# Kernel optimization log

Hardware: AMD Instinct MI355X
Metric: run time of the kernel (lower is better)

Reference implementation:

```python
import jax, jax.numpy as jnp
import numpy as np

D = 512        # input_dim
T = 64         # n_trees
DEPTH = 3
NI = 2 ** DEPTH - 1   # 7 internal nodes
NL = 2 ** DEPTH       # 8 leaves
PPT = NI * D + NI + NL * 2   # params per tree
TOT = PPT * T + T            # + tree_weights
HID = 64


def setup_inputs() -> dict:
    key = jax.random.key(0)
    ks = jax.random.split(key, 10)
    w = lambda k, s: jax.random.normal(k, s, jnp.float32) * 0.05  # xavier-ish small gain
    return {
        "X_train": jax.random.normal(ks[0], (8192, D), jnp.float32),
        "X_test": jax.random.normal(ks[1], (32768, D), jnp.float32),
        "y_train": jax.random.randint(ks[2], (8192,), 0, 2, jnp.int64),
        "W1": w(ks[3], (HID, D)), "b1": jnp.zeros(HID), "g1": jnp.ones(HID), "be1": jnp.zeros(HID),
        "W2": w(ks[4], (HID, HID)), "b2": jnp.zeros(HID),
        "H1": w(ks[5], (2 * HID, HID)), "hb1": jnp.zeros(2 * HID),
        "g2": jnp.ones(2 * HID), "be2": jnp.zeros(2 * HID),
        "H2": w(ks[6], (2 * HID, 2 * HID)), "hb2": jnp.zeros(2 * HID),
        "H3": w(ks[7], (TOT, 2 * HID)), "hb3": jnp.zeros(TOT),
    }


def _ln(x, g, b, eps=1e-5):
    m = x.mean(-1, keepdims=True)
    v = ((x - m) ** 2).mean(-1, keepdims=True)
    return (x - m) / jnp.sqrt(v + eps) * g + b


def reference(X_train, X_test, y_train, W1, b1, g1, be1, W2, b2,
              H1, hb1, g2, be2, H2, hb2, H3, hb3):
    # --- hypernet: data encoder + param generator (Dropout is eval=identity) ---
    h = jax.nn.relu(_ln(X_train @ W1.T + b1, g1, be1))
    h = jax.nn.relu(h @ W2.T + b2)
    c = h.mean(axis=0)                              # [HID] context
    u = jax.nn.relu(_ln(c @ H1.T + hb1, g2, be2))
    u = jax.nn.relu(u @ H2.T + hb2)
    params = u @ H3.T + hb3                         # [TOT]

    # --- parse per-tree params (sequential layout) ---
    rows = params[: T * PPT].reshape(T, PPT)
    sw = rows[:, : NI * D].reshape(T, NI, D)        # split weights
    sb = rows[:, NI * D: NI * D + NI]               # split bias [T, NI]
    ll = rows[:, NI * D + NI:].reshape(T, NL, 2)    # leaf logits
    tw = params[T * PPT:]                           # tree weights [T]

    # --- soft decision trees, all trees/nodes batched ---
    # sigmoid split prob for every (sample, tree, internal node); temperature=1
    p = jax.nn.sigmoid(jnp.einsum('bd,tnd->btn', X_test, sw) + sb[None])  # [B,T,NI]
    B = X_test.shape[0]
    lp = jnp.ones((B, T, 1), X_test.dtype)
    for d in range(DEPTH):                          # unrolled fixed-depth traversal
        s = 2 ** d - 1                              # heap offset of level d
        pd = p[:, :, s: s + 2 ** d]                 # [B,T,2^d]
        lp = jnp.stack([lp * (1 - pd), lp * pd], axis=-1).reshape(B, T, 2 ** (d + 1))
    # original code adds leaf contributions twice (main loop + cleanup loop)
    lp = lp * 2.0                                   # [B,T,NL]

    leaf_dist = jax.nn.softmax(ll, axis=-1)         # [T,NL,2]
    out_t = jnp.einsum('btl,tlc->btc', lp, leaf_dist)
    w = jax.nn.softmax(tw, axis=0)                  # [T]
    return jnp.einsum('btc,t->bc', out_t, w)        # [B,2]
```

## Files before the change

### kernel.cpp

```cpp
#include <hip/hip_runtime.h>
#include <hip/hip_bf16.h>

#define DD 512
#define HIDN 64
#define NTREE 64
#define NIN 7
#define PPTC 3607
#define TOTP 230912
#define SWROWS 448

typedef __attribute__((ext_vector_type(8))) short bf16x8;
typedef __attribute__((ext_vector_type(4))) float f32x4;
typedef __attribute__((ext_vector_type(8))) _Float16 h16x8;

__device__ __forceinline__ unsigned short f2bf(float f) {
  unsigned u = __float_as_uint(f);
  unsigned r = (u + 0x7FFFu + ((u >> 16) & 1u)) >> 16;
  return (unsigned short)r;
}
__device__ __forceinline__ float sigmoidf_(float x) {
  return 1.0f / (1.0f + __expf(-x));
}
__device__ __forceinline__ uint2 pack_bf16x4(float4 v) {
  uint2 pk;
  pk.x = (unsigned)f2bf(v.x) | ((unsigned)f2bf(v.y) << 16);
  pk.y = (unsigned)f2bf(v.z) | ((unsigned)f2bf(v.w) << 16);
  return pk;
}
__device__ __forceinline__ bf16x8 cvt8(float4 a, float4 b) {
  unsigned u0, u1, u2, u3;
  asm("v_cvt_pk_bf16_f32 %0, %1, %2" : "=v"(u0) : "v"(a.x), "v"(a.y));
  asm("v_cvt_pk_bf16_f32 %0, %1, %2" : "=v"(u1) : "v"(a.z), "v"(a.w));
  asm("v_cvt_pk_bf16_f32 %0, %1, %2" : "=v"(u2) : "v"(b.x), "v"(b.y));
  asm("v_cvt_pk_bf16_f32 %0, %1, %2" : "=v"(u3) : "v"(b.z), "v"(b.w));
  union { unsigned u[4]; bf16x8 v; } r;
  r.u[0] = u0; r.u[1] = u1; r.u[2] = u2; r.u[3] = u3;
  return r.v;
}
__device__ __forceinline__ void gl_lds16(const void* g, void* l) {
  __builtin_amdgcn_global_load_lds(
      (const __attribute__((address_space(1))) unsigned int*)g,
      (__attribute__((address_space(3))) unsigned int*)l, 16, 0, 0);
}

__global__ __launch_bounds__(256) void k_train(
    const float* __restrict__ Xtr, const float* __restrict__ W1,
    const float* __restrict__ b1, const float* __restrict__ g1,
    const float* __restrict__ be1, const float* __restrict__ W2,
    const float* __restrict__ b2, float* __restrict__ c_part)
{
  __shared__ __align__(16) char smem[37888];
  char* Xc  = smem;
  char* W1c = smem + 8192;
  char* Hl  = smem + 24576;
  char* W2l = smem + 28672;
  float* lnb = (float*)(smem + 36864);
  float* cp  = (float*)(smem + 37376);

  const int tid = threadIdx.x;
  const int lane = tid & 63;
  const int wv = tid >> 6;
  const int l15 = lane & 15;
  const int gq = lane >> 4;
  const int wm = wv >> 1;
  const int wn = wv & 1;
  const int rb0 = blockIdx.x * 32;

  const float4* X4g = (const float4*)Xtr;
  const float4* W4g = (const float4*)W1;

#pragma unroll
  for (int s = 0; s < 4; ++s) {
    int fidx = tid + s * 256;
    int n = fidx >> 4, kq = fidx & 15;
    float4 v = ((const float4*)W2)[n * 16 + kq];
    uint2 pk = pack_bf16x4(v);
    int off = n * 128 + kq * 8; off ^= (n & 7) << 4;
    *(uint2*)(W2l + off) = pk;
  }

  int xga[4], xo[4];
#pragma unroll
  for (int s = 0; s < 4; ++s) {
    int f = tid + s * 256;
    int m = f >> 5, kq = f & 31;
    xga[s] = (rb0 + m) * 128 + kq;
    xo[s] = (m * 256 + kq * 8) ^ ((m & 7) << 4);
  }
  int wga[8], wo[8];
#pragma unroll
  for (int s = 0; s < 8; ++s) {
    int f = tid + s * 256;
    int n = f >> 5, kq = f & 31;
    wga[s] = n * 128 + kq;
    wo[s] = (n * 256 + kq * 8) ^ ((n & 7) << 4);
  }

  f32x4 acc1[2];
#pragma unroll
  for (int nt = 0; nt < 2; ++nt) { f32x4 z = {0.f,0.f,0.f,0.f}; acc1[nt] = z; }

  float4 xr[4], wr[8];
#pragma unroll
  for (int s = 0; s < 4; ++s) xr[s] = X4g[xga[s]];
#pragma unroll
  for (int s = 0; s < 8; ++s) wr[s] = W4g[wga[s]];

  for (int kc = 0; kc < 4; ++kc) {
    __syncthreads();
#pragma unroll
    for (int s = 0; s < 4; ++s) *(uint2*)(Xc + xo[s]) = pack_bf16x4(xr[s]);
#pragma unroll
    for (int s = 0; s < 8; ++s) *(uint2*)(W1c + wo[s]) = pack_bf16x4(wr[s]);
    if (kc < 3) {
      int ko = (kc + 1) * 32;
#pragma unroll
      for (int s = 0; s < 4; ++s) xr[s] = X4g[xga[s] + ko];
#pragma unroll
      for (int s = 0; s < 8; ++s) wr[s] = W4g[wga[s] + ko];
    }
    __syncthreads();
#pragma unroll
    for (int ks = 0; ks < 4; ++ks) {
      int arow = wm * 16 + l15;
      int aoff = (arow * 256 + ks * 64 + gq * 16) ^ ((arow & 7) << 4);
      bf16x8 afr = *(const bf16x8*)(Xc + aoff);
#pragma unroll
      for (int nt = 0; nt < 2; ++nt) {
        int brow = wn * 32 + nt * 16 + l15;
        int boff = (brow * 256 + ks * 64 + gq * 16) ^ ((brow & 7) << 4);
        bf16x8 bfr = *(const bf16x8*)(W1c + boff);
        acc1[nt] = __builtin_amdgcn_mfma_f32_16x16x32_bf16(afr, bfr, acc1[nt], 0, 0, 0);
      }
    }
  }

  float b1v[2], g1v[2], be1v[2], b2v[2];
#pragma unroll
  for (int nt = 0; nt < 2; ++nt) {
    int c = wn * 32 + nt * 16 + l15;
    b1v[nt] = b1[c]; g1v[nt] = g1[c]; be1v[nt] = be1[c]; b2v[nt] = b2[c];
  }
  float yv[2][4], s_[4], q_[4];
#pragma unroll
  for (int i = 0; i < 4; ++i) {
    float s = 0.f, q = 0.f;
#pragma unroll
    for (int nt = 0; nt < 2; ++nt) {
      float y = acc1[nt][i] + b1v[nt];
      yv[nt][i] = y; s += y; q += y * y;
    }
    s_[i] = s; q_[i] = q;
  }
#pragma unroll
  for (int off = 1; off < 16; off <<= 1) {
#pragma unroll
    for (int i = 0; i < 4; ++i) {
      s_[i] += __shfl_xor(s_[i], off);
      q_[i] += __shfl_xor(q_[i], off);
    }
  }
  if (l15 == 0) {
#pragma unroll
    for (int i = 0; i < 4; ++i) {
      int row = wm * 16 + gq * 4 + i;
      float2 sv; sv.x = s_[i]; sv.y = q_[i];
      *(float2*)(lnb + (row * 2 + wn) * 2) = sv;
    }
  }
  __syncthreads();
#pragma unroll
  for (int i = 0; i < 4; ++i) {
    int row = wm * 16 + gq * 4 + i;
    float2 e0 = *(float2*)(lnb + (row * 2 + 0) * 2);
    float2 e1 = *(float2*)(lnb + (row * 2 + 1) * 2);
    float m = (e0.x + e1.x) * (1.0f / 64.0f);
    float var = (e0.y + e1.y) * (1.0f / 64.0f) - m * m;
    float rstd = rsqrtf(var + 1e-5f);
#pragma unroll
    for (int nt = 0; nt < 2; ++nt) {
      float h = (yv[nt][i] - m) * rstd * g1v[nt] + be1v[nt];
      h = fmaxf(h, 0.0f);
      int col = wn * 32 + nt * 16 + l15;
      int off2 = (row * 128 + col * 2) ^ ((row & 7) << 4);
      *(unsigned short*)(Hl + off2) = f2bf(h);
    }
  }
  __syncthreads();

  f32x4 acc2[2];
#pragma unroll
  for (int nt = 0; nt < 2; ++nt) { f32x4 z = {0.f,0.f,0.f,0.f}; acc2[nt] = z; }
#pragma unroll
  for (int ks = 0; ks < 2; ++ks) {
    int arow = wm * 16 + l15;
    int aoff = (arow * 128 + ks * 64 + gq * 16) ^ ((arow & 7) << 4);
    bf16x8 afr = *(const bf16x8*)(Hl + aoff);
#pragma unroll
    for (int nt = 0; nt < 2; ++nt) {
      int brow = wn * 32 + nt * 16 + l15;
      int boff = (brow * 128 + ks * 64 + gq * 16) ^ ((brow & 7) << 4);
      bf16x8 bfr = *(const bf16x8*)(W2l + boff);
      acc2[nt] = __builtin_amdgcn_mfma_f32_16x16x32_bf16(afr, bfr, acc2[nt], 0, 0, 0);
    }
  }
  float cs[2];
#pragma unroll
  for (int nt = 0; nt < 2; ++nt) {
    float s = 0.f;
#pragma unroll
    for (int i = 0; i < 4; ++i) s += fmaxf(acc2[nt][i] + b2v[nt], 0.0f);
    cs[nt] = s;
  }
#pragma unroll
  for (int nt = 0; nt < 2; ++nt) {
    cs[nt] += __shfl_xor(cs[nt], 16);
    cs[nt] += __shfl_xor(cs[nt], 32);
  }
  if (lane < 16) {
#pragma unroll
    for (int nt = 0; nt < 2; ++nt)
      cp[wm * 64 + wn * 32 + nt * 16 + lane] = cs[nt];
  }
  __syncthreads();
  if (tid < 64) c_part[blockIdx.x * 64 + tid] = cp[tid] + cp[64 + tid];
}

__global__ __launch_bounds__(256) void k_head(
    const float* __restrict__ c_part,
    const float* __restrict__ H1, const float* __restrict__ hb1,
    const float* __restrict__ g2, const float* __restrict__ be2,
    const float* __restrict__ H2, const float* __restrict__ hb2,
    float* __restrict__ u2out)
{
  __shared__ float part[256];
  __shared__ float clds[64];
  __shared__ float u1lds[128];
  __shared__ float red[8];
  int tid = threadIdx.x;
  {
    int col = tid & 63, g = tid >> 6;
    float s0 = 0.f, s1 = 0.f, s2 = 0.f, s3 = 0.f;
    int b0 = g * 64;
    for (int b = 0; b < 64; b += 4) {
      s0 += c_part[(b0 + b + 0) * 64 + col];
      s1 += c_part[(b0 + b + 1) * 64 + col];
      s2 += c_part[(b0 + b + 2) * 64 + col];
      s3 += c_part[(b0 + b + 3) * 64 + col];
    }
    part[tid] = (s0 + s1) + (s2 + s3);
  }
  __syncthreads();
  if (tid < 64)
    clds[tid] = (part[tid] + part[64 + tid] + part[128 + tid] + part[192 + tid]) * (1.0f / 8192.0f);
  __syncthreads();
  float acc = 0.f;
  if (tid < 128) {
    float a0 = 0.f, a1 = 0.f, a2 = 0.f, a3 = 0.f;
    for (int k = 0; k < 64; k += 4) {
      a0 += clds[k + 0] * H1[tid * 64 + k + 0];
      a1 += clds[k + 1] * H1[tid * 64 + k + 1];
      a2 += clds[k + 2] * H1[tid * 64 + k + 2];
      a3 += clds[k + 3] * H1[tid * 64 + k + 3];
    }
    acc = hb1[tid] + ((a0 + a1) + (a2 + a3));
  }
  float s = acc, q = acc * acc;
#pragma unroll
  for (int off = 1; off < 64; off <<= 1) { s += __shfl_xor(s, off); q += __shfl_xor(q, off); }
  int wv = tid >> 6;
  if ((tid & 63) == 0) { red[wv * 2] = s; red[wv * 2 + 1] = q; }
  __syncthreads();
  float S = red[0] + red[2], Q = red[1] + red[3];
  float m = S * (1.0f / 128.0f);
  float var = Q * (1.0f / 128.0f) - m * m;
  float rstd = rsqrtf(var + 1e-5f);
  if (tid < 128)
    u1lds[tid] = fmaxf((acc - m) * rstd * g2[tid] + be2[tid], 0.0f);
  __syncthreads();
  if (tid < 128) {
    float c0 = 0.f, c1 = 0.f, c2 = 0.f, c3 = 0.f;
    for (int k = 0; k < 128; k += 4) {
      c0 += u1lds[k + 0] * H2[tid * 128 + k + 0];
      c1 += u1lds[k + 1] * H2[tid * 128 + k + 1];
      c2 += u1lds[k + 2] * H2[tid * 128 + k + 2];
      c3 += u1lds[k + 3] * H2[tid * 128 + k + 3];
    }
    u2out[tid] = fmaxf(hb2[tid] + ((c0 + c1) + (c2 + c3)), 0.0f);
  }
}

__global__ __launch_bounds__(256) void k_params(
    const float* __restrict__ H3, const float* __restrict__ hb3,
    const float* __restrict__ u2,
    unsigned short* __restrict__ Bfrag, float* __restrict__ sb,
    float* __restrict__ ll, float* __restrict__ tw)
{
  __shared__ float u2l[128];
  int tid = threadIdx.x;
  if (tid < 128) u2l[tid] = u2[tid];
  __syncthreads();
  int row = blockIdx.x * 64 + (tid >> 2);
  int sub = tid & 3;
  float acc = 0.0f;
  const float4* H4 = (const float4*)H3;
#pragma unroll
  for (int j = 0; j < 8; ++j) {
    int f = j * 4 + sub;
    float4 v = H4[row * 32 + f];
    acc += v.x * u2l[f * 4] + v.y * u2l[f * 4 + 1] + v.z * u2l[f * 4 + 2] + v.w * u2l[f * 4 + 3];
  }
  acc += __shfl_xor(acc, 1);
  acc += __shfl_xor(acc, 2);
  if (sub == 0) {
    float val = acc + hb3[row];
    if (row >= 230848) {
      tw[row - 230848] = val;
    } else {
      int t = row / PPTC;
      int r = row - t * PPTC;
      if (r < 3584) {
        int n = r >> 9, d = r & 511;
        int col = t * 7 + n;
        int kt = d >> 5, gq = (d >> 3) & 3, j = d & 7;
        Bfrag[kt * 16384 + col * 32 + (gq ^ (col & 3)) * 8 + j] = f2bf(val);
      } else if (r < 3591) {
        sb[t * 7 + (r - 3584)] = val;
      } else {
        ll[t * 16 + (r - 3591)] = val;
      }
    }
  }
}

__global__ __launch_bounds__(512) void k_test(
    const float* __restrict__ Xt, const unsigned short* __restrict__ Bfrag,
    const float* __restrict__ sb, const float* __restrict__ ll,
    const float* __restrict__ tw, float* __restrict__ out)
{
  __shared__ __align__(16) char smem[154368];
  char* Pl = smem;
  float* qlds = (float*)(smem + 147456);
  float* sbl  = (float*)(smem + 151552);
  float* outl = (float*)(smem + 153344);

  const int tid = threadIdx.x;
  const int lane = tid & 63;
  const int wv = tid >> 6;
  const int l15 = lane & 15;
  const int gq = lane >> 4;
  const int wm = wv >> 2;
  const int wn = wv & 3;
  const int bm0 = blockIdx.x * 128;

  const float4* X4 = (const float4*)Xt;
  const char* Bf = (const char*)Bfrag;

  if (tid < 448) sbl[tid] = sb[tid];
  if (tid < 64) {
    int t = tid;
    float x = tw[t];
    float m = x;
#pragma unroll
    for (int off = 1; off < 64; off <<= 1) m = fmaxf(m, __shfl_xor(m, off));
    float e = __expf(x - m);
    float s = e;
#pragma unroll
    for (int off = 1; off < 64; off <<= 1) s += __shfl_xor(s, off);
    float w = e / s;
#pragma unroll
    for (int l = 0; l < 8; ++l) {
      float a = ll[t * 16 + l * 2], b = ll[t * 16 + l * 2 + 1];
      float mm = fmaxf(a, b);
      float e0 = __expf(a - mm), e1 = __expf(b - mm);
      float inv = 2.0f * w / (e0 + e1);
      qlds[t * 16 + l * 2] = e0 * inv;
      qlds[t * 16 + l * 2 + 1] = e1 * inv;
    }
  }

  const int xrow0 = tid >> 3;
  const int xpg   = (tid & 7) ^ (xrow0 & 7);
  const int xsrc0 = (bm0 + xrow0) * 128 + xpg;
  const int xsrc1 = (bm0 + xrow0 + 64) * 128 + xpg;

#define ISSUE_TILE(t_) do { \
    char* xb_ = smem + ((t_) % 3) * 49152; \
    char* bb_ = xb_ + 16384; \
    gl_lds16(X4 + (xsrc0 + (t_) * 8), xb_ + tid * 16); \
    gl_lds16(X4 + (xsrc1 + (t_) * 8), xb_ + (tid + 512) * 16); \
    const char* bt_ = Bf + (t_) * 32768; \
    gl_lds16(bt_ + tid * 16,          bb_ + tid * 16); \
    gl_lds16(bt_ + (tid + 512) * 16,  bb_ + (tid + 512) * 16); \
    gl_lds16(bt_ + (tid + 1024) * 16, bb_ + (tid + 1024) * 16); \
    gl_lds16(bt_ + (tid + 1536) * 16, bb_ + (tid + 1536) * 16); \
  } while (0)

  f32x4 acc[4][7];
#pragma unroll
  for (int mt = 0; mt < 4; ++mt)
#pragma unroll
    for (int nt = 0; nt < 7; ++nt) { f32x4 z = {0.f,0.f,0.f,0.f}; acc[mt][nt] = z; }

  const int xoff0 = (((gq * 2) ^ (l15 & 7)) << 4);
  const int xoff1 = (((gq * 2 + 1) ^ (l15 & 7)) << 4);
  int arow[4];
#pragma unroll
  for (int mt = 0; mt < 4; ++mt) arow[mt] = (wm * 64 + mt * 16 + l15) * 128;
  const int bxor = ((gq ^ (l15 & 3)) << 4);
  int boffs[7];
#pragma unroll
  for (int nt = 0; nt < 7; ++nt) boffs[nt] = (wn * 112 + nt * 16 + l15) * 64 + bxor;

#define COMPUTE_TILE(t_) do { \
    char* xb_ = smem + ((t_) % 3) * 49152; \
    char* bb_ = xb_ + 16384; \
    bf16x8 abf[4]; \
    _Pragma("unroll") \
    for (int mt = 0; mt < 4; ++mt) { \
      float4 a0 = *(const float4*)(xb_ + arow[mt] + xoff0); \
      float4 a1 = *(const float4*)(xb_ + arow[mt] + xoff1); \
      abf[mt] = cvt8(a0, a1); \
    } \
    _Pragma("unroll") \
    for (int nt = 0; nt < 7; ++nt) { \
      bf16x8 bfr = *(const bf16x8*)(bb_ + boffs[nt]); \
      _Pragma("unroll") \
      for (int mt = 0; mt < 4; ++mt) \
        acc[mt][nt] = __builtin_amdgcn_mfma_f32_16x16x32_bf16(abf[mt], bfr, acc[mt][nt], 0, 0, 0); \
    } } while (0)

  ISSUE_TILE(0);
  ISSUE_TILE(1);
  ISSUE_TILE(2);
  asm volatile("s_waitcnt lgkmcnt(0)" ::: "memory");

  for (int t = 0; t < 13; ++t) {
    asm volatile("s_waitcnt vmcnt(12)" ::: "memory");
    __builtin_amdgcn_sched_barrier(0);
    __builtin_amdgcn_s_barrier();
    COMPUTE_TILE(t);
    __builtin_amdgcn_s_barrier();
    ISSUE_TILE(t + 3);
  }
  asm volatile("s_waitcnt vmcnt(12)" ::: "memory");
  __builtin_amdgcn_sched_barrier(0);
  __builtin_amdgcn_s_barrier();
  COMPUTE_TILE(13);
  __builtin_amdgcn_s_barrier();
  asm volatile("s_waitcnt vmcnt(6)" ::: "memory");
  __builtin_amdgcn_sched_barrier(0);
  __builtin_amdgcn_s_barrier();
  COMPUTE_TILE(14);
  __builtin_amdgcn_s_barrier();
  asm volatile("s_waitcnt vmcnt(0)" ::: "memory");
  __builtin_amdgcn_sched_barrier(0);
  __builtin_amdgcn_s_barrier();
  COMPUTE_TILE(15);
  __syncthreads();

  float qreg[16];
  {
    const float4* q4 = (const float4*)qlds;
#pragma unroll
    for (int j = 0; j < 4; ++j) {
      float4 v = q4[lane * 4 + j];
      qreg[j * 4] = v.x; qreg[j * 4 + 1] = v.y; qreg[j * 4 + 2] = v.z; qreg[j * 4 + 3] = v.w;
    }
  }

#pragma unroll
  for (int rg = 0; rg < 4; ++rg) {
    if (wm == (rg >> 1)) {
#pragma unroll
      for (int mtl = 0; mtl < 2; ++mtl) {
        const int mt = (rg & 1) * 2 + mtl;
#pragma unroll
        for (int nt = 0; nt < 7; ++nt) {
          int col = wn * 112 + nt * 16 + l15;
          float sbv = sbl[col];
          int t = col / 7;
          int j = col - t * 7;
          int slot2 = (t * 8 + j) * 2;
#pragma unroll
          for (int i = 0; i < 4; ++i) {
            int rl = mtl * 16 + gq * 4 + i;
            float p = sigmoidf_(acc[mt][nt][i] + sbv);
            *(_Float16*)(Pl + rl * 1024 + slot2) = (_Float16)p;
          }
        }
      }
    }
    __syncthreads();
#pragma unroll
    for (int k = 0; k < 4; ++k) {
      int rl = wv * 4 + k;
      h16x8 v = *(const h16x8*)(Pl + rl * 1024 + lane * 16);
      float p0 = (float)v[0], p1 = (float)v[1], p2 = (float)v[2];
      float p3 = (float)v[3], p4 = (float)v[4], p5 = (float)v[5], p6 = (float)v[6];
      float n0 = 1.f - p0, n1 = 1.f - p1, n2 = 1.f - p2;
      float a00 = n0 * n1, a01 = n0 * p1, a10 = p0 * n2, a11 = p0 * p2;
      float L0 = a00 * (1.f - p3), L1 = a00 * p3;
      float L2 = a01 * (1.f - p4), L3 = a01 * p4;
      float L4 = a10 * (1.f - p5), L5 = a10 * p5;
      float L6 = a11 * (1.f - p6), L7 = a11 * p6;
      float o0 = L0*qreg[0] + L1*qreg[2] + L2*qreg[4] + L3*qreg[6]
               + L4*qreg[8] + L5*qreg[10] + L6*qreg[12] + L7*qreg[14];
      float o1 = L0*qreg[1] + L1*qreg[3] + L2*qreg[5] + L3*qreg[7]
               + L4*qreg[9] + L5*qreg[11] + L6*qreg[13] + L7*qreg[15];
#pragma unroll
      for (int off = 1; off < 64; off <<= 1) {
        o0 += __shfl_xor(o0, off);
        o1 += __shfl_xor(o1, off);
      }
      if (lane == 0) {
        int gr = rg * 32 + rl;
        outl[gr * 2] = o0;
        outl[gr * 2 + 1] = o1;
      }
    }
    __syncthreads();
  }
  if (tid < 256) out[bm0 * 2 + tid] = outl[tid];
#undef ISSUE_TILE
#undef COMPUTE_TILE
}

extern "C" void kernel_launch(void* const* d_in, const int* in_sizes, int n_in,
                              void* d_out, int out_size, void* d_ws, size_t ws_size,
                              hipStream_t stream)
{
  const float* Xtr = (const float*)d_in[0];
  const float* Xte = (const float*)d_in[1];
  const float* W1  = (const float*)d_in[3];
  const float* b1  = (const float*)d_in[4];
  const float* g1  = (const float*)d_in[5];
  const float* be1 = (const float*)d_in[6];
  const float* W2  = (const float*)d_in[7];
  const float* b2  = (const float*)d_in[8];
  const float* H1  = (const float*)d_in[9];
  const float* hb1 = (const float*)d_in[10];
  const float* g2  = (const float*)d_in[11];
  const float* be2 = (const float*)d_in[12];
  const float* H2  = (const float*)d_in[13];
  const float* hb2 = (const float*)d_in[14];
  const float* H3  = (const float*)d_in[15];
  const float* hb3 = (const float*)d_in[16];
  float* out = (float*)d_out;
  char* ws = (char*)d_ws;

  float* c_part = (float*)ws;
  float* u2     = (float*)(ws + 65536);
  float* sb     = (float*)(ws + 66048);
  float* ll     = (float*)(ws + 67840);
  float* tw     = (float*)(ws + 71936);
  unsigned short* Bfrag = (unsigned short*)(ws + 72192);

  k_train<<<256, 256, 0, stream>>>(Xtr, W1, b1, g1, be1, W2, b2, c_part);
  k_head<<<1, 256, 0, stream>>>(c_part, H1, hb1, g2, be2, H2, hb2, u2);
  k_params<<<3608, 256, 0, stream>>>(H3, hb3, u2, Bfrag, sb, ll, tw);
  k_test<<<256, 512, 0, stream>>>(Xte, Bfrag, sb, ll, tw, out);
}
```

Before: 84.53 us.

## Split test GEMM across tree halves with atomic output accumulation

The test kernel now splits the 448 split-node columns into two halves of 32 trees each. It launches 512 blocks of 256 threads instead of 256 blocks of 512, with a smaller double-buffered LDS footprint so two blocks can share a CU. Each block atomically adds its partial per-sample outputs into a buffer zeroed in k_params, and the B fragment layout is reorganised per half. The aim is better occupancy and CU balance, at the cost of reading X twice, atomic traffic, and a shallower prefetch pipeline.

```diff
diff --git a/kernel.cpp b/kernel.cpp
--- a/kernel.cpp
+++ b/kernel.cpp
@@ -294,11 +294,13 @@
     const float* __restrict__ H3, const float* __restrict__ hb3,
     const float* __restrict__ u2,
     unsigned short* __restrict__ Bfrag, float* __restrict__ sb,
-    float* __restrict__ ll, float* __restrict__ tw)
+    float* __restrict__ ll, float* __restrict__ tw,
+    float* __restrict__ outz)
 {
   __shared__ float u2l[128];
   int tid = threadIdx.x;
   if (tid < 128) u2l[tid] = u2[tid];
+  if (blockIdx.x < 256) outz[blockIdx.x * 256 + tid] = 0.0f;
   __syncthreads();
   int row = blockIdx.x * 64 + (tid >> 2);
   int sub = tid & 3;
@@ -321,9 +323,10 @@
       int r = row - t * PPTC;
       if (r < 3584) {
         int n = r >> 9, d = r & 511;
-        int col = t * 7 + n;
-        int kt = d >> 5, gq = (d >> 3) & 3, j = d & 7;
-        Bfrag[kt * 16384 + col * 32 + (gq ^ (col & 3)) * 8 + j] = f2bf(val);
+        int half = t >> 5;
+        int colp = (t & 31) * 7 + n;
+        int kt = d >> 5, kgq = (d >> 3) & 3, j = d & 7;
+        Bfrag[(half * 16 + kt) * 8192 + (kgq * 256 + colp) * 8 + j] = f2bf(val);
       } else if (r < 3591) {
         sb[t * 7 + (r - 3584)] = val;
       } else {
@@ -333,30 +336,33 @@
   }
 }
 
-__global__ __launch_bounds__(512) void k_test(
+__global__ __launch_bounds__(256, 2) void k_test(
     const float* __restrict__ Xt, const unsigned short* __restrict__ Bfrag,
     const float* __restrict__ sb, const float* __restrict__ ll,
     const float* __restrict__ tw, float* __restrict__ out)
 {
-  __shared__ __align__(16) char smem[154368];
+  __shared__ __align__(16) char smem[68608];
   char* Pl = smem;
-  float* qlds = (float*)(smem + 147456);
-  float* sbl  = (float*)(smem + 151552);
-  float* outl = (float*)(smem + 153344);
+  float* qlds = (float*)(smem + 65536);
+  float* sbl  = (float*)(smem + 67584);
 
   const int tid = threadIdx.x;
   const int lane = tid & 63;
   const int wv = tid >> 6;
   const int l15 = lane & 15;
   const int gq = lane >> 4;
-  const int wm = wv >> 2;
-  const int wn = wv & 3;
-  const int bm0 = blockIdx.x * 128;
+  const int wm = wv >> 1;
+  const int wn = wv & 1;
+  const int bx = blockIdx.x;
+  const int mblk = (bx >> 4) * 8 + (bx & 7);
+  const int half = (bx >> 3) & 1;
+  const int bm0 = mblk * 128;
+  const int T0 = half * 32;
 
   const float4* X4 = (const float4*)Xt;
-  const char* Bf = (const char*)Bfrag;
-
-  if (tid < 448) sbl[tid] = sb[tid];
+  const char* Bf = (const char*)Bfrag + half * 262144;
+
+  if (tid < 224) sbl[tid] = sb[T0 * 7 + tid];
   if (tid < 64) {
     int t = tid;
     float x = tw[t];
@@ -368,32 +374,40 @@
 #pragma unroll
     for (int off = 1; off < 64; off <<= 1) s += __shfl_xor(s, off);
     float w = e / s;
-#pragma unroll
-    for (int l = 0; l < 8; ++l) {
-      float a = ll[t * 16 + l * 2], b = ll[t * 16 + l * 2 + 1];
-      float mm = fmaxf(a, b);
-      float e0 = __expf(a - mm), e1 = __expf(b - mm);
-      float inv = 2.0f * w / (e0 + e1);
-      qlds[t * 16 + l * 2] = e0 * inv;
-      qlds[t * 16 + l * 2 + 1] = e1 * inv;
-    }
-  }
-
-  const int xrow0 = tid >> 3;
-  const int xpg   = (tid & 7) ^ (xrow0 & 7);
-  const int xsrc0 = (bm0 + xrow0) * 128 + xpg;
-  const int xsrc1 = (bm0 + xrow0 + 64) * 128 + xpg;
+    if ((t >> 5) == half) {
+      int lt = t & 31;
+#pragma unroll
+      for (int l = 0; l < 8; ++l) {
+        float a = ll[t * 16 + l * 2], b = ll[t * 16 + l * 2 + 1];
+        float mm = fmaxf(a, b);
+        float e0 = __expf(a - mm), e1 = __expf(b - mm);
+        float inv = 2.0f * w / (e0 + e1);
+        qlds[lt * 16 + l * 2] = e0 * inv;
+        qlds[lt * 16 + l * 2 + 1] = e1 * inv;
+      }
+    }
+  }
+
+  int xsrc[4];
+#pragma unroll
+  for (int s = 0; s < 4; ++s) {
+    int row = (tid >> 3) + s * 32;
+    int pg = (tid & 7) ^ (row & 7);
+    xsrc[s] = (bm0 + row) * 128 + pg;
+  }
 
 #define ISSUE_TILE(t_) do { \
-    char* xb_ = smem + ((t_) % 3) * 49152; \
+    char* xb_ = smem + ((t_) & 1) * 32768; \
     char* bb_ = xb_ + 16384; \
-    gl_lds16(X4 + (xsrc0 + (t_) * 8), xb_ + tid * 16); \
-    gl_lds16(X4 + (xsrc1 + (t_) * 8), xb_ + (tid + 512) * 16); \
-    const char* bt_ = Bf + (t_) * 32768; \
+    gl_lds16(X4 + (xsrc[0] + (t_) * 8), xb_ + tid * 16); \
+    gl_lds16(X4 + (xsrc[1] + (t_) * 8), xb_ + (tid + 256) * 16); \
+    gl_lds16(X4 + (xsrc[2] + (t_) * 8), xb_ + (tid + 512) * 16); \
+    gl_lds16(X4 + (xsrc[3] + (t_) * 8), xb_ + (tid + 768) * 16); \
+    const char* bt_ = Bf + (t_) * 16384; \
     gl_lds16(bt_ + tid * 16,          bb_ + tid * 16); \
+    gl_lds16(bt_ + (tid + 256) * 16,  bb_ + (tid + 256) * 16); \
     gl_lds16(bt_ + (tid + 512) * 16,  bb_ + (tid + 512) * 16); \
-    gl_lds16(bt_ + (tid + 1024) * 16, bb_ + (tid + 1024) * 16); \
-    gl_lds16(bt_ + (tid + 1536) * 16, bb_ + (tid + 1536) * 16); \
+    gl_lds16(bt_ + (tid + 768) * 16,  bb_ + (tid + 768) * 16); \
   } while (0)
 
   f32x4 acc[4][7];
@@ -402,18 +416,18 @@
 #pragma unroll
     for (int nt = 0; nt < 7; ++nt) { f32x4 z = {0.f,0.f,0.f,0.f}; acc[mt][nt] = z; }
 
-  const int xoff0 = (((gq * 2) ^ (l15 & 7)) << 4);
-  const int xoff1 = (((gq * 2 + 1) ^ (l15 & 7)) << 4);
+  const int xoff0 = (((2 * gq) ^ (l15 & 7)) << 4);
+  const int xoff1 = (((2 * gq + 1) ^ (l15 & 7)) << 4);
   int arow[4];
 #pragma unroll
   for (int mt = 0; mt < 4; ++mt) arow[mt] = (wm * 64 + mt * 16 + l15) * 128;
-  const int bxor = ((gq ^ (l15 & 3)) << 4);
   int boffs[7];
 #pragma unroll
-  for (int nt = 0; nt < 7; ++nt) boffs[nt] = (wn * 112 + nt * 16 + l15) * 64 + bxor;
+  for (int nt = 0; nt < 7; ++nt)
+    boffs[nt] = (gq * 256 + wn * 112 + nt * 16 + l15) * 16;
 
 #define COMPUTE_TILE(t_) do { \
-    char* xb_ = smem + ((t_) % 3) * 49152; \
+    char* xb_ = smem + ((t_) & 1) * 32768; \
     char* bb_ = xb_ + 16384; \
     bf16x8 abf[4]; \
     _Pragma("unroll") \
@@ -432,27 +446,17 @@
 
   ISSUE_TILE(0);
   ISSUE_TILE(1);
-  ISSUE_TILE(2);
   asm volatile("s_waitcnt lgkmcnt(0)" ::: "memory");
 
-  for (int t = 0; t < 13; ++t) {
-    asm volatile("s_waitcnt vmcnt(12)" ::: "memory");
+#pragma unroll 1
+  for (int t = 0; t < 15; ++t) {
+    asm volatile("s_waitcnt vmcnt(8)" ::: "memory");
     __builtin_amdgcn_sched_barrier(0);
     __builtin_amdgcn_s_barrier();
     COMPUTE_TILE(t);
     __builtin_amdgcn_s_barrier();
-    ISSUE_TILE(t + 3);
-  }
-  asm volatile("s_waitcnt vmcnt(12)" ::: "memory");
-  __builtin_amdgcn_sched_barrier(0);
-  __builtin_amdgcn_s_barrier();
-  COMPUTE_TILE(13);
-  __builtin_amdgcn_s_barrier();
-  asm volatile("s_waitcnt vmcnt(6)" ::: "memory");
-  __builtin_amdgcn_sched_barrier(0);
-  __builtin_amdgcn_s_barrier();
-  COMPUTE_TILE(14);
-  __builtin_amdgcn_s_barrier();
+    if (t < 14) ISSUE_TILE(t + 2);
+  }
   asm volatile("s_waitcnt vmcnt(0)" ::: "memory");
   __builtin_amdgcn_sched_barrier(0);
   __builtin_amdgcn_s_barrier();
@@ -462,10 +466,15 @@
   float qreg[16];
   {
     const float4* q4 = (const float4*)qlds;
+    int lt = lane & 31;
 #pragma unroll
     for (int j = 0; j < 4; ++j) {
-      float4 v = q4[lane * 4 + j];
-      qreg[j * 4] = v.x; qreg[j * 4 + 1] = v.y; qreg[j * 4 + 2] = v.z; qreg[j * 4 + 3] = v.w;
+      float4 v = q4[lt * 4 + j];
+      bool lo = (lane < 32);
+      qreg[j * 4]     = lo ? v.x : 0.f;
+      qreg[j * 4 + 1] = lo ? v.y : 0.f;
+      qreg[j * 4 + 2] = lo ? v.z : 0.f;
+      qreg[j * 4 + 3] = lo ? v.w : 0.f;
     }
   }
 
@@ -479,23 +488,23 @@
         for (int nt = 0; nt < 7; ++nt) {
           int col = wn * 112 + nt * 16 + l15;
           float sbv = sbl[col];
-          int t = col / 7;
-          int j = col - t * 7;
-          int slot2 = (t * 8 + j) * 2;
+          int lt = col / 7;
+          int jj = col - lt * 7;
+          int slot2 = (lt * 8 + jj) * 2;
 #pragma unroll
           for (int i = 0; i < 4; ++i) {
             int rl = mtl * 16 + gq * 4 + i;
             float p = sigmoidf_(acc[mt][nt][i] + sbv);
-            *(_Float16*)(Pl + rl * 1024 + slot2) = (_Float16)p;
+            *(_Float16*)(Pl + rl * 512 + slot2) = (_Float16)p;
           }
         }
       }
     }
     __syncthreads();
 #pragma unroll
-    for (int k = 0; k < 4; ++k) {
-      int rl = wv * 4 + k;
-      h16x8 v = *(const h16x8*)(Pl + rl * 1024 + lane * 16);
+    for (int k = 0; k < 8; ++k) {
+      int rl = wv * 8 + k;
+      h16x8 v = *(const h16x8*)(Pl + rl * 512 + (lane & 31) * 16);
       float p0 = (float)v[0], p1 = (float)v[1], p2 = (float)v[2];
       float p3 = (float)v[3], p4 = (float)v[4], p5 = (float)v[5], p6 = (float)v[6];
       float n0 = 1.f - p0, n1 = 1.f - p1, n2 = 1.f - p2;
@@ -514,14 +523,13 @@
         o1 += __shfl_xor(o1, off);
       }
       if (lane == 0) {
-        int gr = rg * 32 + rl;
-        outl[gr * 2] = o0;
-        outl[gr * 2 + 1] = o1;
+        int gr = bm0 + rg * 32 + rl;
+        atomicAdd(&out[gr * 2], o0);
+        atomicAdd(&out[gr * 2 + 1], o1);
       }
     }
     __syncthreads();
   }
-  if (tid < 256) out[bm0 * 2 + tid] = outl[tid];
 #undef ISSUE_TILE
 #undef COMPUTE_TILE
 }
@@ -558,6 +566,6 @@
 
   k_train<<<256, 256, 0, stream>>>(Xtr, W1, b1, g1, be1, W2, b2, c_part);
   k_head<<<1, 256, 0, stream>>>(c_part, H1, hb1, g2, be2, H2, hb2, u2);
-  k_params<<<3608, 256, 0, stream>>>(H3, hb3, u2, Bfrag, sb, ll, tw);
-  k_test<<<256, 512, 0, stream>>>(Xte, Bfrag, sb, ll, tw, out);
-}
+  k_params<<<3608, 256, 0, stream>>>(H3, hb3, u2, Bfrag, sb, ll, tw, out);
+  k_test<<<512, 256, 0, stream>>>(Xte, Bfrag, sb, ll, tw, out);
+}
```

New measurement: 93.09 us. 1.1x slower.

## Convert X tiles to bf16 once in registers and restage through LDS double buffer

Applied to the files above, without the earlier changes.

X test tiles used to be copied into LDS as fp32 with direct global-to-LDS loads, and each wave converted them to bf16 at every read. Now each thread loads X into registers, converts once, and writes a bf16 tile into a double-buffered LDS region, while B tiles stay triple-buffered with direct loads. The B-fragment swizzle in the producer kernel changes to match the new XOR pattern. This cuts LDS footprint and redundant conversion work, but adds register-staged loads, more barriers per tile, and a more complex hand-scheduled pipeline.

```diff
diff --git a/kernel.cpp b/kernel.cpp
--- a/kernel.cpp
+++ b/kernel.cpp
@@ -27,15 +27,12 @@
   pk.y = (unsigned)f2bf(v.z) | ((unsigned)f2bf(v.w) << 16);
   return pk;
 }
-__device__ __forceinline__ bf16x8 cvt8(float4 a, float4 b) {
-  unsigned u0, u1, u2, u3;
+__device__ __forceinline__ uint2 cvtpk2(float4 a) {
+  unsigned u0, u1;
   asm("v_cvt_pk_bf16_f32 %0, %1, %2" : "=v"(u0) : "v"(a.x), "v"(a.y));
   asm("v_cvt_pk_bf16_f32 %0, %1, %2" : "=v"(u1) : "v"(a.z), "v"(a.w));
-  asm("v_cvt_pk_bf16_f32 %0, %1, %2" : "=v"(u2) : "v"(b.x), "v"(b.y));
-  asm("v_cvt_pk_bf16_f32 %0, %1, %2" : "=v"(u3) : "v"(b.z), "v"(b.w));
-  union { unsigned u[4]; bf16x8 v; } r;
-  r.u[0] = u0; r.u[1] = u1; r.u[2] = u2; r.u[3] = u3;
-  return r.v;
+  uint2 r; r.x = u0; r.y = u1;
+  return r;
 }
 __device__ __forceinline__ void gl_lds16(const void* g, void* l) {
   __builtin_amdgcn_global_load_lds(
@@ -322,8 +319,8 @@
       if (r < 3584) {
         int n = r >> 9, d = r & 511;
         int col = t * 7 + n;
-        int kt = d >> 5, gq = (d >> 3) & 3, j = d & 7;
-        Bfrag[kt * 16384 + col * 32 + (gq ^ (col & 3)) * 8 + j] = f2bf(val);
+        int kt = d >> 5, kgq = (d >> 3) & 3, j = d & 7;
+        Bfrag[kt * 16384 + col * 32 + (kgq ^ ((col >> 1) & 3)) * 8 + j] = f2bf(val);
       } else if (r < 3591) {
         sb[t * 7 + (r - 3584)] = val;
       } else {
@@ -338,11 +335,13 @@
     const float* __restrict__ sb, const float* __restrict__ ll,
     const float* __restrict__ tw, float* __restrict__ out)
 {
-  __shared__ __align__(16) char smem[154368];
+  __shared__ __align__(16) char smem[121600];
   char* Pl = smem;
-  float* qlds = (float*)(smem + 147456);
-  float* sbl  = (float*)(smem + 151552);
-  float* outl = (float*)(smem + 153344);
+  char* Xb0 = smem + 98304;
+  char* Xb1 = smem + 106496;
+  float* qlds = (float*)(smem + 114688);
+  float* sbl  = (float*)(smem + 118784);
+  float* outl = (float*)(smem + 120576);
 
   const int tid = threadIdx.x;
   const int lane = tid & 63;
@@ -379,22 +378,24 @@
     }
   }
 
-  const int xrow0 = tid >> 3;
-  const int xpg   = (tid & 7) ^ (xrow0 & 7);
-  const int xsrc0 = (bm0 + xrow0) * 128 + xpg;
-  const int xsrc1 = (bm0 + xrow0 + 64) * 128 + xpg;
-
-#define ISSUE_TILE(t_) do { \
-    char* xb_ = smem + ((t_) % 3) * 49152; \
-    char* bb_ = xb_ + 16384; \
-    gl_lds16(X4 + (xsrc0 + (t_) * 8), xb_ + tid * 16); \
-    gl_lds16(X4 + (xsrc1 + (t_) * 8), xb_ + (tid + 512) * 16); \
-    const char* bt_ = Bf + (t_) * 32768; \
-    gl_lds16(bt_ + tid * 16,          bb_ + tid * 16); \
-    gl_lds16(bt_ + (tid + 512) * 16,  bb_ + (tid + 512) * 16); \
-    gl_lds16(bt_ + (tid + 1024) * 16, bb_ + (tid + 1024) * 16); \
-    gl_lds16(bt_ + (tid + 1536) * 16, bb_ + (tid + 1536) * 16); \
-  } while (0)
+  const int xr_ = tid >> 3;
+  const int xq_ = tid & 7;
+  const int xsrc0 = (bm0 + xr_) * 128 + xq_;
+  const int xsrc1 = (bm0 + xr_ + 64) * 128 + xq_;
+  const int xwo0 = xr_ * 64 + (((xq_ >> 1) ^ ((xr_ >> 1) & 3)) << 4) + (xq_ & 1) * 8;
+
+  int aoffs[4];
+#pragma unroll
+  for (int mt = 0; mt < 4; ++mt) {
+    int row = wm * 64 + mt * 16 + l15;
+    aoffs[mt] = row * 64 + ((gq ^ ((row >> 1) & 3)) << 4);
+  }
+  int boffs[7];
+#pragma unroll
+  for (int nt = 0; nt < 7; ++nt) {
+    int col = wn * 112 + nt * 16 + l15;
+    boffs[nt] = col * 64 + ((gq ^ ((col >> 1) & 3)) << 4);
+  }
 
   f32x4 acc[4][7];
 #pragma unroll
@@ -402,61 +403,90 @@
 #pragma unroll
     for (int nt = 0; nt < 7; ++nt) { f32x4 z = {0.f,0.f,0.f,0.f}; acc[mt][nt] = z; }
 
-  const int xoff0 = (((gq * 2) ^ (l15 & 7)) << 4);
-  const int xoff1 = (((gq * 2 + 1) ^ (l15 & 7)) << 4);
-  int arow[4];
-#pragma unroll
-  for (int mt = 0; mt < 4; ++mt) arow[mt] = (wm * 64 + mt * 16 + l15) * 128;
-  const int bxor = ((gq ^ (l15 & 3)) << 4);
-  int boffs[7];
-#pragma unroll
-  for (int nt = 0; nt < 7; ++nt) boffs[nt] = (wn * 112 + nt * 16 + l15) * 64 + bxor;
-
-#define COMPUTE_TILE(t_) do { \
-    char* xb_ = smem + ((t_) % 3) * 49152; \
-    char* bb_ = xb_ + 16384; \
+#define LOADX(kt, a_, b_) do { \
+    a_ = X4[xsrc0 + (kt) * 8]; b_ = X4[xsrc1 + (kt) * 8]; } while (0)
+#define WRITEX(Xb, a_, b_) do { \
+    *(uint2*)((Xb) + xwo0) = cvtpk2(a_); \
+    *(uint2*)((Xb) + xwo0 + 4096) = cvtpk2(b_); } while (0)
+#define ISSUEB(bb, kt) do { \
+    const char* bt_ = Bf + (kt) * 32768; \
+    gl_lds16(bt_ + tid * 16,          (bb) + tid * 16); \
+    gl_lds16(bt_ + tid * 16 + 8192,   (bb) + tid * 16 + 8192); \
+    gl_lds16(bt_ + tid * 16 + 16384,  (bb) + tid * 16 + 16384); \
+    gl_lds16(bt_ + tid * 16 + 24576,  (bb) + tid * 16 + 24576); } while (0)
+#define COMPUTE(Xb, Bb) do { \
     bf16x8 abf[4]; \
     _Pragma("unroll") \
-    for (int mt = 0; mt < 4; ++mt) { \
-      float4 a0 = *(const float4*)(xb_ + arow[mt] + xoff0); \
-      float4 a1 = *(const float4*)(xb_ + arow[mt] + xoff1); \
-      abf[mt] = cvt8(a0, a1); \
-    } \
+    for (int mt = 0; mt < 4; ++mt) abf[mt] = *(const bf16x8*)((Xb) + aoffs[mt]); \
     _Pragma("unroll") \
     for (int nt = 0; nt < 7; ++nt) { \
-      bf16x8 bfr = *(const bf16x8*)(bb_ + boffs[nt]); \
+      bf16x8 bfr = *(const bf16x8*)((Bb) + boffs[nt]); \
       _Pragma("unroll") \
       for (int mt = 0; mt < 4; ++mt) \
         acc[mt][nt] = __builtin_amdgcn_mfma_f32_16x16x32_bf16(abf[mt], bfr, acc[mt][nt], 0, 0, 0); \
     } } while (0)
-
-  ISSUE_TILE(0);
-  ISSUE_TILE(1);
-  ISSUE_TILE(2);
-  asm volatile("s_waitcnt lgkmcnt(0)" ::: "memory");
-
-  for (int t = 0; t < 13; ++t) {
-    asm volatile("s_waitcnt vmcnt(12)" ::: "memory");
+#define VMWAIT(n) do { \
+    asm volatile("s_waitcnt vmcnt(" #n ")" ::: "memory"); \
+    __builtin_amdgcn_sched_barrier(0); } while (0)
+#define LGKM0_BAR() do { \
+    asm volatile("s_waitcnt lgkmcnt(0)" ::: "memory"); \
+    __builtin_amdgcn_s_barrier(); } while (0)
+
+  char* bb0 = smem;
+  char* bb1 = smem + 32768;
+  char* bb2 = smem + 65536;
+
+  float4 xrA0, xrA1;
+  float4 xrB0, xrB1;
+
+  ISSUEB(bb0, 0);
+  LOADX(0, xrA0, xrA1);
+  __builtin_amdgcn_sched_barrier(0);
+  ISSUEB(bb1, 1);
+  LOADX(1, xrB0, xrB1);
+  __builtin_amdgcn_sched_barrier(0);
+  ISSUEB(bb2, 2);
+  VMWAIT(10);
+  WRITEX(Xb0, xrA0, xrA1);
+  LGKM0_BAR();
+
+#pragma unroll 1
+  for (int i = 0; i < 6; ++i) {
+    const int t = 2 * i;
+    COMPUTE(Xb0, bb0);
+    VMWAIT(4);
+    WRITEX(Xb1, xrB0, xrB1);
+    LGKM0_BAR();
+    LOADX(t + 2, xrA0, xrA1);
     __builtin_amdgcn_sched_barrier(0);
-    __builtin_amdgcn_s_barrier();
-    COMPUTE_TILE(t);
-    __builtin_amdgcn_s_barrier();
-    ISSUE_TILE(t + 3);
-  }
-  asm volatile("s_waitcnt vmcnt(12)" ::: "memory");
+    ISSUEB(bb0, t + 3);
+    COMPUTE(Xb1, bb1);
+    VMWAIT(4);
+    WRITEX(Xb0, xrA0, xrA1);
+    LGKM0_BAR();
+    LOADX(t + 3, xrB0, xrB1);
+    __builtin_amdgcn_sched_barrier(0);
+    ISSUEB(bb1, t + 4);
+    char* tmp = bb0; bb0 = bb2; bb2 = bb1; bb1 = tmp;
+  }
+  COMPUTE(Xb0, bb0);
+  VMWAIT(4);
+  WRITEX(Xb1, xrB0, xrB1);
+  LGKM0_BAR();
+  LOADX(14, xrA0, xrA1);
   __builtin_amdgcn_sched_barrier(0);
-  __builtin_amdgcn_s_barrier();
-  COMPUTE_TILE(13);
-  __builtin_amdgcn_s_barrier();
-  asm volatile("s_waitcnt vmcnt(6)" ::: "memory");
+  ISSUEB(bb0, 15);
+  COMPUTE(Xb1, bb1);
+  VMWAIT(4);
+  WRITEX(Xb0, xrA0, xrA1);
+  LGKM0_BAR();
+  LOADX(15, xrB0, xrB1);
   __builtin_amdgcn_sched_barrier(0);
-  __builtin_amdgcn_s_barrier();
-  COMPUTE_TILE(14);
-  __builtin_amdgcn_s_barrier();
-  asm volatile("s_waitcnt vmcnt(0)" ::: "memory");
-  __builtin_amdgcn_sched_barrier(0);
-  __builtin_amdgcn_s_barrier();
-  COMPUTE_TILE(15);
+  COMPUTE(Xb0, bb2);
+  VMWAIT(0);
+  WRITEX(Xb1, xrB0, xrB1);
+  LGKM0_BAR();
+  COMPUTE(Xb1, bb0);
   __syncthreads();
 
   float qreg[16];
@@ -522,8 +552,12 @@
     __syncthreads();
   }
   if (tid < 256) out[bm0 * 2 + tid] = outl[tid];
-#undef ISSUE_TILE
-#undef COMPUTE_TILE
+#undef LOADX
+#undef WRITEX
+#undef ISSUEB
+#undef COMPUTE
+#undef VMWAIT
+#undef LGKM0_BAR
 }
 
 extern "C" void kernel_launch(void* const* d_in, const int* in_sizes, int n_in,
```

Result: faster. 81.26 us, median of 3 (-3.9%).
